# Kernel optimization log

Measured on AMD Instinct MI355X. Metric: run time of the kernel, lower is better.

## Reference

```python
import jax, jax.numpy as jnp
import numpy as np
import math

N_HEAD = 16

def setup_inputs() -> dict:
    key = jax.random.key(0)
    ks = jax.random.split(key, 8)
    B, S, P, NX = 4, 1024, 128, 1024
    return {
        "x": jax.random.normal(ks[0], (B, S, NX), jnp.float32),
        "M": jax.random.normal(ks[1], (B, P, NX), jnp.float32),
        "Mmask": jnp.ones((B, P), jnp.float32),
        "attention_mask": jnp.zeros((B, 1, 1, S), jnp.float32),
        "W_attn": jax.random.normal(ks[2], (NX, 3 * NX), jnp.float32) * 0.02,
        "b_attn": jnp.zeros((3 * NX,), jnp.float32),
        "W_mem": jax.random.normal(ks[3], (NX, 2 * NX), jnp.float32) * 0.02,
        "b_mem": jnp.zeros((2 * NX,), jnp.float32),
        "W_proj": jax.random.normal(ks[4], (NX, NX), jnp.float32) * 0.02,
        "b_proj": jnp.zeros((NX,), jnp.float32),
    }

def _split_heads(t, H):
    B, T, NX = t.shape
    return t.reshape(B, T, H, NX // H).transpose(0, 2, 1, 3)  # [B,H,T,dh]

def reference(x, M, Mmask, attention_mask, W_attn, b_attn, W_mem, b_mem, W_proj, b_proj):
    B, S, NX = x.shape
    H = N_HEAD
    dh = NX // H
    P = M.shape[1]

    # fused QKV projection (Conv1D == x @ W + b)
    qkv = x @ W_attn + b_attn
    q, k, v = jnp.split(qkv, 3, axis=2)

    # memory K/V projection, prepended along the key/value sequence axis
    ekv = M @ W_mem + b_mem
    ek, ev = jnp.split(ekv, 2, axis=2)
    key = jnp.concatenate([ek, k], axis=1)   # [B, P+S, NX]
    value = jnp.concatenate([ev, v], axis=1)

    qh = _split_heads(q, H)      # [B,H,S,dh]
    kh = _split_heads(key, H)    # [B,H,P+S,dh]
    vh = _split_heads(value, H)  # [B,H,P+S,dh]

    w = jnp.einsum('bhsd,bhtd->bhst', qh, kh) / math.sqrt(dh)  # [B,H,S,P+S]

    # causal bias over the self part, all-ones over the memory part
    causal = jnp.tril(jnp.ones((S, S), w.dtype))
    b = jnp.concatenate([jnp.ones((S, P), w.dtype), causal], axis=1)[None, None]  # [1,1,S,P+S]
    w = w * b - 10000.0 * (1.0 - b)

    # additive attention mask: memory-mask bias concatenated before token mask
    mem_bias = (1.0 - Mmask)[:, None, None, :] * -10000.0  # [B,1,1,P]
    am = jnp.concatenate([mem_bias, jnp.broadcast_to(attention_mask, (B, 1, 1, S))], axis=3)
    w = w + am

    w = jax.nn.softmax(w, axis=-1)
    a = jnp.einsum('bhst,bhtd->bhsd', w, vh)                  # [B,H,S,dh]
    a = a.transpose(0, 2, 1, 3).reshape(B, S, NX)             # merge heads
    return a @ W_proj + b_proj
```

## Files before the change

### kernel.cpp

```cpp
#include <hip/hip_runtime.h>
#include <hip/hip_bf16.h>


typedef __attribute__((ext_vector_type(8))) short bf16x8;
typedef __attribute__((ext_vector_type(4))) float f32x4;

#define MFMA16(a, b, c) __builtin_amdgcn_mfma_f32_16x16x32_bf16((a), (b), (c), 0, 0, 0)

#define GLOAD_LDS16(g, l)                                                  \
    __builtin_amdgcn_global_load_lds(                                      \
        (const __attribute__((address_space(1))) void*)(const void*)(g),   \
        (__attribute__((address_space(3))) void*)(void*)(l), 16, 0, 0)

static __device__ __forceinline__ unsigned short f2bf(float f) {
    union { float f; unsigned int u; } v; v.f = f;
    unsigned int u = v.u;
    return (unsigned short)((u + 0x7fffu + ((u >> 16) & 1u)) >> 16);
}

static __device__ __forceinline__ void transpose_body(const float* __restrict__ W,
                                                      unsigned short* __restrict__ Wt,
                                                      int K, int N, int bx, int by,
                                                      float (*tile)[33]) {
    int n0 = bx * 32, k0 = by * 32;
    int tx = threadIdx.x & 31, ty = threadIdx.x >> 5;
    #pragma unroll
    for (int r = ty; r < 32; r += 8) tile[r][tx] = W[(size_t)(k0 + r) * N + n0 + tx];
    __syncthreads();
    #pragma unroll
    for (int r = ty; r < 32; r += 8) Wt[(size_t)(n0 + r) * K + k0 + tx] = f2bf(tile[tx][r]);
}

__global__ void prep_all(const float* __restrict__ x, const float* __restrict__ Mem,
                         unsigned short* __restrict__ x_bf, unsigned short* __restrict__ M_bf,
                         const float* __restrict__ W_attn, const float* __restrict__ W_mem,
                         const float* __restrict__ W_proj, unsigned short* __restrict__ Wat,
                         unsigned short* __restrict__ Wmt, unsigned short* __restrict__ Wpt,
                         const float* __restrict__ Mmask, const float* __restrict__ amask,
                         float* __restrict__ biasT) {
    __shared__ float tile[32][33];
    int bid = blockIdx.x;
    if (bid < 4608) {
        int i = bid * 256 + threadIdx.x;
        if (i < 1048576) {
            float4 v = ((const float4*)x)[i];
            ushort4 o; o.x = f2bf(v.x); o.y = f2bf(v.y); o.z = f2bf(v.z); o.w = f2bf(v.w);
            ((ushort4*)x_bf)[i] = o;
        } else {
            int j = i - 1048576;
            float4 v = ((const float4*)Mem)[j];
            ushort4 o; o.x = f2bf(v.x); o.y = f2bf(v.y); o.z = f2bf(v.z); o.w = f2bf(v.w);
            ((ushort4*)M_bf)[j] = o;
        }
        return;
    }
    bid -= 4608;
    if (bid < 3072) {
        transpose_body(W_attn, Wat, 1024, 3072, bid % 96, bid / 96, tile);
    } else if (bid < 5120) {
        int t = bid - 3072; transpose_body(W_mem, Wmt, 1024, 2048, t % 64, t / 64, tile);
    } else if (bid < 6144) {
        int t = bid - 5120; transpose_body(W_proj, Wpt, 1024, 1024, t % 32, t / 32, tile);
    } else {
        int i = (bid - 6144) * 256 + threadIdx.x;
        if (i < 4 * 1152) {
            int b = i / 1152, t = i % 1152;
            float v = (t < 128) ? (Mmask[b * 128 + t] - 1.f) * 10000.f
                                : amask[b * 1024 + t - 128];
            biasT[i] = v * 1.4426950408889634f;
        }
    }
}

__global__ __launch_bounds__(256, 4) void gemm_fused(
        const unsigned short* __restrict__ x_bf, const unsigned short* __restrict__ Wat,
        const float* __restrict__ b_attn, const unsigned short* __restrict__ M_bf,
        const unsigned short* __restrict__ Wmt, const float* __restrict__ b_mem,
        unsigned short* __restrict__ Qbuf, unsigned short* __restrict__ Kc,
        unsigned short* __restrict__ Vt) {
    __shared__ char smem[34816];
    unsigned short* As = (unsigned short*)smem;
    unsigned short* Bs = (unsigned short*)(smem + 8192);
    const int tid = threadIdx.x;
    const int lane = tid & 63, wave = tid >> 6;
    const int quad = lane >> 4, l16 = lane & 15;
    const int crow = lane >> 2, ccol = (lane & 3) * 8;
    const int bid = blockIdx.x;

    if (bid < 768) {
        const int bm = bid & 31, bn = bid >> 5;
        const int wm = (wave & 1) * 64, wn = (wave >> 1) * 64;
        const unsigned short* Abase = x_bf + (size_t)(bm * 128 + crow) * 1024 + ccol;
        const unsigned short* Bbase = Wat + (size_t)(bn * 128 + crow) * 1024 + ccol;
        f32x4 acc[4][4] = {};
        for (int k0 = 0; k0 < 1024; k0 += 32) {
            __syncthreads();
            #pragma unroll
            for (int cc = 0; cc < 4; cc++) {
                const int c = wave * 4 + cc;
                if (c < 8) GLOAD_LDS16(Abase + (size_t)(c * 16) * 1024 + k0, &As[c * 512]);
                else       GLOAD_LDS16(Bbase + (size_t)((c - 8) * 16) * 1024 + k0, &Bs[(c - 8) * 512]);
            }
            __syncthreads();
            bf16x8 af[4], bf[4];
            #pragma unroll
            for (int i = 0; i < 4; i++) af[i] = *(const bf16x8*)&As[(wm + i * 16 + l16) * 32 + quad * 8];
            #pragma unroll
            for (int j = 0; j < 4; j++) bf[j] = *(const bf16x8*)&Bs[(wn + j * 16 + l16) * 32 + quad * 8];
            #pragma unroll
            for (int i = 0; i < 4; i++)
                #pragma unroll
                for (int j = 0; j < 4; j++)
                    acc[i][j] = MFMA16(af[i], bf[j], acc[i][j]);
        }
        float bj[4];
        #pragma unroll
        for (int j = 0; j < 4; j++) bj[j] = b_attn[bn * 128 + wn + j * 16 + l16];
        __syncthreads();
        if (bn < 8) {
            #pragma unroll
            for (int i = 0; i < 4; i++) {
                const int row = bm * 128 + wm + i * 16 + quad * 4;
                #pragma unroll
                for (int j = 0; j < 4; j++) {
                    const int col = bn * 128 + wn + j * 16 + l16;
                    #pragma unroll
                    for (int r = 0; r < 4; r++)
                        Qbuf[(size_t)(row + r) * 1024 + col] = f2bf(acc[i][j][r] + bj[j]);
                }
            }
        } else if (bn < 16) {
            #pragma unroll
            for (int i = 0; i < 4; i++) {
                const int row = bm * 128 + wm + i * 16 + quad * 4;
                const int b = row >> 10, s = row & 1023;
                #pragma unroll
                for (int j = 0; j < 4; j++) {
                    const int c = bn * 128 + wn + j * 16 + l16 - 1024;
                    unsigned short* kd = Kc + (size_t)((b << 4) | (c >> 6)) * 73728 +
                                         (size_t)(s + 128) * 64 + (c & 63);
                    #pragma unroll
                    for (int r = 0; r < 4; r++) kd[(size_t)r * 64] = f2bf(acc[i][j][r] + bj[j]);
                }
            }
        } else {
            unsigned short* Tw = (unsigned short*)smem + wave * 4352;
            #pragma unroll
            for (int i = 0; i < 4; i++)
                #pragma unroll
                for (int j = 0; j < 4; j++)
                    #pragma unroll
                    for (int r = 0; r < 4; r++)
                        Tw[(j * 16 + l16) * 68 + i * 16 + quad * 4 + r] = f2bf(acc[i][j][r] + bj[j]);
            const int vb = (bn - 16) * 128 + wn;
            const int h = vb >> 6;
            const int b = bm >> 3, s0 = (bm * 128 + wm) & 1023;
            unsigned short* vd = Vt + (size_t)((b << 4) | h) * 73728 +
                                 (size_t)lane * 1152 + 128 + s0;
            #pragma unroll
            for (int ch = 0; ch < 8; ch++)
                *(bf16x8*)(vd + ch * 8) = *(const bf16x8*)&Tw[lane * 68 + ch * 8];
        }
    } else {
        const int t = bid - 768;
        const int bm = t >> 5, bn = t & 31;
        const int wm = (wave & 1) * 32, wn = (wave >> 1) * 32;
        const unsigned short* Abase = M_bf + (size_t)(bm * 64 + crow) * 1024 + ccol;
        const unsigned short* Bbase = Wmt + (size_t)(bn * 64 + crow) * 1024 + ccol;
        f32x4 acc[2][2] = {};
        for (int k0 = 0; k0 < 1024; k0 += 32) {
            __syncthreads();
            #pragma unroll
            for (int cc = 0; cc < 2; cc++) {
                const int c = wave * 2 + cc;
                if (c < 4) GLOAD_LDS16(Abase + (size_t)(c * 16) * 1024 + k0, &As[c * 512]);
                else       GLOAD_LDS16(Bbase + (size_t)((c - 4) * 16) * 1024 + k0, &Bs[(c - 4) * 512]);
            }
            __syncthreads();
            bf16x8 af[2], bf[2];
            #pragma unroll
            for (int i = 0; i < 2; i++) af[i] = *(const bf16x8*)&As[(wm + i * 16 + l16) * 32 + quad * 8];
            #pragma unroll
            for (int j = 0; j < 2; j++) bf[j] = *(const bf16x8*)&Bs[(wn + j * 16 + l16) * 32 + quad * 8];
            #pragma unroll
            for (int i = 0; i < 2; i++)
                #pragma unroll
                for (int j = 0; j < 2; j++)
                    acc[i][j] = MFMA16(af[i], bf[j], acc[i][j]);
        }
        float bj[2];
        #pragma unroll
        for (int j = 0; j < 2; j++) bj[j] = b_mem[bn * 64 + wn + j * 16 + l16];
        __syncthreads();
        if (bn < 16) {
            #pragma unroll
            for (int i = 0; i < 2; i++) {
                const int row = bm * 64 + wm + i * 16 + quad * 4;
                const int b = row >> 7, p = row & 127;
                #pragma unroll
                for (int j = 0; j < 2; j++) {
                    const int c = bn * 64 + wn + j * 16 + l16;
                    unsigned short* kd = Kc + (size_t)((b << 4) | (c >> 6)) * 73728 +
                                         (size_t)p * 64 + (c & 63);
                    #pragma unroll
                    for (int r = 0; r < 4; r++) kd[(size_t)r * 64] = f2bf(acc[i][j][r] + bj[j]);
                }
            }
        } else {
            unsigned short* Tw = (unsigned short*)smem + wave * 1152;
            #pragma unroll
            for (int i = 0; i < 2; i++)
                #pragma unroll
                for (int j = 0; j < 2; j++)
                    #pragma unroll
                    for (int r = 0; r < 4; r++)
                        Tw[(j * 16 + l16) * 36 + i * 16 + quad * 4 + r] = f2bf(acc[i][j][r] + bj[j]);
            const int vb = bn * 64 + wn - 1024;
            const int h = vb >> 6, d0 = vb & 63;
            const int b = (bm * 64 + wm) >> 7, p0 = (bm * 64 + wm) & 127;
            const int lc = lane >> 1, half = lane & 1;
            unsigned short* vd = Vt + (size_t)((b << 4) | h) * 73728 +
                                 (size_t)(d0 + lc) * 1152 + p0 + half * 16;
            #pragma unroll
            for (int ch = 0; ch < 2; ch++)
                *(bf16x8*)(vd + ch * 8) = *(const bf16x8*)&Tw[lc * 36 + half * 16 + ch * 8];
        }
    }
}

__global__ __launch_bounds__(256) void attn_kernel(const unsigned short* __restrict__ Qbuf,
                                                   const unsigned short* __restrict__ Kc,
                                                   const unsigned short* __restrict__ Vt,
                                                   const float* __restrict__ biasT,
                                                   unsigned short* __restrict__ Aout) {
    __shared__ unsigned short Ks[2 * 64 * 32];
    __shared__ unsigned short Vs[2 * 64 * 32];
    __shared__ unsigned short Ps[4][16 * 72];
    const int tid = threadIdx.x;
    const int lane = tid & 63, wave = tid >> 6;
    const int quad = lane >> 4, l16 = lane & 15;
    const int blk = blockIdx.x;
    const int xcd = blk & 7, idx = blk >> 3;
    const int bh = xcd * 8 + (idx >> 4);
    const int qg = 15 - (idx & 15);
    const int h = bh & 15, b = bh >> 4;
    const int qrow0 = qg * 64;
    const int qrow_w = qrow0 + wave * 16;

    bf16x8 qf[2];
    #pragma unroll
    for (int k2 = 0; k2 < 2; k2++)
        qf[k2] = *(const bf16x8*)(Qbuf + (size_t)(b * 1024 + qrow_w + l16) * 1024 +
                                  h * 64 + k2 * 32 + quad * 8);

    const unsigned short* Kb = Kc + (size_t)bh * 73728;
    const unsigned short* Vb = Vt + (size_t)bh * 73728;
    const float* bias_b = biasT + b * 1152;

    const int srow = lane >> 2;
    const int sc8 = (lane & 3) * 8;

    bf16x8 ones;
    #pragma unroll
    for (int j = 0; j < 8; j++) ones[j] = (short)0x3F80;

    f32x4 o[4] = {};
    f32x4 oden = {};
    const int tmax = min(1152, qrow0 + 192);

    for (int t0 = 0; t0 < tmax; t0 += 64) {
        __syncthreads();
        #pragma unroll
        for (int cc = 0; cc < 4; cc++) {
            const int c = wave * 4 + cc;
            if (c < 8) {
                const int kk = c & 1, rch = c >> 1;
                GLOAD_LDS16(Kb + (size_t)(t0 + rch * 16 + srow) * 64 + kk * 32 + sc8,
                            &Ks[kk * 2048 + rch * 512]);
            } else {
                const int c2 = c - 8, tk = c2 & 1, dch = c2 >> 1;
                GLOAD_LDS16(Vb + (size_t)(dch * 16 + srow) * 1152 + t0 + tk * 32 + sc8,
                            &Vs[tk * 2048 + dch * 512]);
            }
        }
        __syncthreads();
        if (t0 <= qrow_w + 143) {
            const bool nomask = (t0 + 63 <= 128 + qrow_w);
            float4 bt[4];
            #pragma unroll
            for (int tn = 0; tn < 4; tn++)
                bt[tn] = *(const float4*)(bias_b + t0 + tn * 16 + quad * 4);
            const int sg = qrow_w + l16;
            #pragma unroll
            for (int tn = 0; tn < 4; tn++) {
                bf16x8 kf0 = *(const bf16x8*)&Ks[0 * 2048 + (tn * 16 + l16) * 32 + quad * 8];
                bf16x8 kf1 = *(const bf16x8*)&Ks[1 * 2048 + (tn * 16 + l16) * 32 + quad * 8];
                f32x4 st = {};
                st = MFMA16(kf0, qf[0], st);
                st = MFMA16(kf1, qf[1], st);
                float p[4];
                #pragma unroll
                for (int r = 0; r < 4; r++) {
                    float e = __builtin_amdgcn_exp2f(st[r] * 0.18033688011112042f + bt[tn][r]);
                    if (!nomask) {
                        const int tg = t0 + tn * 16 + quad * 4 + r;
                        e = (tg < 128 || tg - 128 <= sg) ? e : 0.f;
                    }
                    p[r] = e;
                }
                union { ushort4 u; __hip_bfloat162 h2[2]; } pk;
                pk.h2[0] = __float22bfloat162_rn(float2{p[0], p[1]});
                pk.h2[1] = __float22bfloat162_rn(float2{p[2], p[3]});
                *(ushort4*)&Ps[wave][l16 * 72 + tn * 16 + quad * 4] = pk.u;
            }
            #pragma unroll
            for (int tk = 0; tk < 2; tk++) {
                bf16x8 pf = *(const bf16x8*)&Ps[wave][l16 * 72 + tk * 32 + quad * 8];
                oden = MFMA16(pf, ones, oden);
                #pragma unroll
                for (int dn = 0; dn < 4; dn++) {
                    bf16x8 vf = *(const bf16x8*)&Vs[tk * 2048 + (dn * 16 + l16) * 32 + quad * 8];
                    o[dn] = MFMA16(pf, vf, o[dn]);
                }
            }
        }
    }

    #pragma unroll
    for (int r = 0; r < 4; r++) {
        const float inv = 1.f / oden[r];
        const size_t orow = (size_t)(b * 1024 + qrow_w + quad * 4 + r) * 1024 + h * 64;
        #pragma unroll
        for (int dn = 0; dn < 4; dn++)
            Aout[orow + dn * 16 + l16] = f2bf(o[dn][r] * inv);
    }
}

__global__ __launch_bounds__(256) void gemm_proj(const unsigned short* __restrict__ Abuf,
                                                 const unsigned short* __restrict__ Wpt,
                                                 const float* __restrict__ b_proj,
                                                 float* __restrict__ out) {
    __shared__ unsigned short As[128 * 32];
    __shared__ unsigned short Bs[64 * 32];
    const int tid = threadIdx.x;
    const int lane = tid & 63, wave = tid >> 6;
    const int quad = lane >> 4, l16 = lane & 15;
    const int wm = (wave & 1) * 64, wn = (wave >> 1) * 32;
    const int bm = blockIdx.x & 31, bn = blockIdx.x >> 5;
    const int crow = lane >> 2, ccol = (lane & 3) * 8;
    const unsigned short* Abase = Abuf + (size_t)(bm * 128 + crow) * 1024 + ccol;
    const unsigned short* Bbase = Wpt + (size_t)(bn * 64 + crow) * 1024 + ccol;

    f32x4 acc[4][2] = {};
    for (int k0 = 0; k0 < 1024; k0 += 32) {
        __syncthreads();
        #pragma unroll
        for (int cc = 0; cc < 3; cc++) {
            const int c = wave * 3 + cc;
            if (c < 8) GLOAD_LDS16(Abase + (size_t)(c * 16) * 1024 + k0, &As[c * 512]);
            else if (c < 12) GLOAD_LDS16(Bbase + (size_t)((c - 8) * 16) * 1024 + k0, &Bs[(c - 8) * 512]);
        }
        __syncthreads();
        bf16x8 af[4], bf[2];
        #pragma unroll
        for (int i = 0; i < 4; i++) af[i] = *(const bf16x8*)&As[(wm + i * 16 + l16) * 32 + quad * 8];
        #pragma unroll
        for (int j = 0; j < 2; j++) bf[j] = *(const bf16x8*)&Bs[(wn + j * 16 + l16) * 32 + quad * 8];
        #pragma unroll
        for (int i = 0; i < 4; i++)
            #pragma unroll
            for (int j = 0; j < 2; j++)
                acc[i][j] = MFMA16(af[i], bf[j], acc[i][j]);
    }
    float bj[2];
    #pragma unroll
    for (int j = 0; j < 2; j++) bj[j] = b_proj[bn * 64 + wn + j * 16 + l16];
    #pragma unroll
    for (int i = 0; i < 4; i++) {
        const int row = bm * 128 + wm + i * 16 + quad * 4;
        #pragma unroll
        for (int j = 0; j < 2; j++) {
            const int col = bn * 64 + wn + j * 16 + l16;
            #pragma unroll
            for (int r = 0; r < 4; r++)
                out[(size_t)(row + r) * 1024 + col] = acc[i][j][r] + bj[j];
        }
    }
}

extern "C" void kernel_launch(void* const* d_in, const int* in_sizes, int n_in,
                              void* d_out, int out_size, void* d_ws, size_t ws_size,
                              hipStream_t stream) {
    const float* x      = (const float*)d_in[0];
    const float* Mem    = (const float*)d_in[1];
    const float* Mmask  = (const float*)d_in[2];
    const float* amask  = (const float*)d_in[3];
    const float* W_attn = (const float*)d_in[4];
    const float* b_attn = (const float*)d_in[5];
    const float* W_mem  = (const float*)d_in[6];
    const float* b_mem  = (const float*)d_in[7];
    const float* W_proj = (const float*)d_in[8];
    const float* b_proj = (const float*)d_in[9];
    float* out = (float*)d_out;

    char* ws = (char*)d_ws;
    unsigned short* x_bf  = (unsigned short*)ws;  ws += (size_t)4096 * 1024 * 2;
    unsigned short* M_bf  = (unsigned short*)ws;  ws += (size_t)512 * 1024 * 2;
    unsigned short* Wat   = (unsigned short*)ws;  ws += (size_t)3072 * 1024 * 2;
    unsigned short* Wmt   = (unsigned short*)ws;  ws += (size_t)2048 * 1024 * 2;
    unsigned short* Wpt   = (unsigned short*)ws;  ws += (size_t)1024 * 1024 * 2;
    unsigned short* Qbuf  = (unsigned short*)ws;  ws += (size_t)4096 * 1024 * 2;
    unsigned short* Abuf  = (unsigned short*)ws;  ws += (size_t)4096 * 1024 * 2;
    unsigned short* Kc    = (unsigned short*)ws;  ws += (size_t)64 * 1152 * 64 * 2;
    unsigned short* Vt    = (unsigned short*)ws;  ws += (size_t)64 * 64 * 1152 * 2;
    float*          biasT = (float*)ws;           ws += (size_t)4 * 1152 * 4;

    prep_all<<<10771, 256, 0, stream>>>(x, Mem, x_bf, M_bf, W_attn, W_mem, W_proj,
                                        Wat, Wmt, Wpt, Mmask, amask, biasT);
    gemm_fused<<<1024, 256, 0, stream>>>(x_bf, Wat, b_attn, M_bf, Wmt, b_mem,
                                         Qbuf, Kc, Vt);
    attn_kernel<<<1024, 256, 0, stream>>>(Qbuf, Kc, Vt, biasT, Abuf);
    gemm_proj<<<512, 256, 0, stream>>>(Abuf, Wpt, b_proj, out);
}
```

Before: 209.4 us.

## Shrink attention blocks to two waves with paired causal query tiles and swizzled LDS

The attention kernel now launches 128-thread blocks, each handling two 32-row query tiles from opposite ends of the causal range (pair and 31-pair), so per-block work is balanced. K/V tiles are loaded whole by one wave each into 64x64 LDS arrays with an XOR swizzle on the column chunk to avoid bank conflicts. Smaller blocks raise occupancy but halve the reuse of each K/V tile across query rows, so more global/LDS traffic per query.

```diff
diff --git a/kernel.cpp b/kernel.cpp
--- a/kernel.cpp
+++ b/kernel.cpp
@@ -228,111 +228,116 @@
     }
 }
 
-__global__ __launch_bounds__(256) void attn_kernel(const unsigned short* __restrict__ Qbuf,
+__global__ __launch_bounds__(128) void attn_kernel(const unsigned short* __restrict__ Qbuf,
                                                    const unsigned short* __restrict__ Kc,
                                                    const unsigned short* __restrict__ Vt,
                                                    const float* __restrict__ biasT,
                                                    unsigned short* __restrict__ Aout) {
-    __shared__ unsigned short Ks[2 * 64 * 32];
-    __shared__ unsigned short Vs[2 * 64 * 32];
-    __shared__ unsigned short Ps[4][16 * 72];
+    __shared__ unsigned short Ks[64 * 64];
+    __shared__ unsigned short Vs[64 * 64];
+    __shared__ unsigned short Ps[2][16 * 72];
     const int tid = threadIdx.x;
     const int lane = tid & 63, wave = tid >> 6;
     const int quad = lane >> 4, l16 = lane & 15;
     const int blk = blockIdx.x;
     const int xcd = blk & 7, idx = blk >> 3;
-    const int bh = xcd * 8 + (idx >> 4);
-    const int qg = 15 - (idx & 15);
+    const int bh = xcd * 8 + (idx & 7);
+    const int pair = idx >> 3;
     const int h = bh & 15, b = bh >> 4;
-    const int qrow0 = qg * 64;
-    const int qrow_w = qrow0 + wave * 16;
-
-    bf16x8 qf[2];
-    #pragma unroll
-    for (int k2 = 0; k2 < 2; k2++)
-        qf[k2] = *(const bf16x8*)(Qbuf + (size_t)(b * 1024 + qrow_w + l16) * 1024 +
-                                  h * 64 + k2 * 32 + quad * 8);
 
     const unsigned short* Kb = Kc + (size_t)bh * 73728;
     const unsigned short* Vb = Vt + (size_t)bh * 73728;
     const float* bias_b = biasT + b * 1152;
 
-    const int srow = lane >> 2;
-    const int sc8 = (lane & 3) * 8;
+    const int srow = lane >> 3;
+    const int scol = ((lane & 7) ^ srow) * 8;
+    const int rswz = l16 & 7;
 
     bf16x8 ones;
     #pragma unroll
     for (int j = 0; j < 8; j++) ones[j] = (short)0x3F80;
 
-    f32x4 o[4] = {};
-    f32x4 oden = {};
-    const int tmax = min(1152, qrow0 + 192);
-
-    for (int t0 = 0; t0 < tmax; t0 += 64) {
-        __syncthreads();
-        #pragma unroll
-        for (int cc = 0; cc < 4; cc++) {
-            const int c = wave * 4 + cc;
-            if (c < 8) {
-                const int kk = c & 1, rch = c >> 1;
-                GLOAD_LDS16(Kb + (size_t)(t0 + rch * 16 + srow) * 64 + kk * 32 + sc8,
-                            &Ks[kk * 2048 + rch * 512]);
+    #pragma unroll
+    for (int phase = 0; phase < 2; phase++) {
+        const int qg = phase ? (31 - pair) : pair;
+        const int qrow0 = qg * 32;
+        const int qrow_w = qrow0 + wave * 16;
+
+        bf16x8 qf[2];
+        #pragma unroll
+        for (int k2 = 0; k2 < 2; k2++)
+            qf[k2] = *(const bf16x8*)(Qbuf + (size_t)(b * 1024 + qrow_w + l16) * 1024 +
+                                      h * 64 + k2 * 32 + quad * 8);
+
+        f32x4 o[4] = {};
+        f32x4 oden = {};
+        const int tmax = min(1152, ((qrow0 + 223) >> 6) << 6);
+
+        for (int t0 = 0; t0 < tmax; t0 += 64) {
+            __syncthreads();
+            if (wave == 0) {
+                const unsigned short* g = Kb + (size_t)(t0 + srow) * 64 + scol;
+                #pragma unroll
+                for (int ch = 0; ch < 8; ch++)
+                    GLOAD_LDS16(g + (size_t)(ch * 8) * 64, &Ks[ch * 512]);
             } else {
-                const int c2 = c - 8, tk = c2 & 1, dch = c2 >> 1;
-                GLOAD_LDS16(Vb + (size_t)(dch * 16 + srow) * 1152 + t0 + tk * 32 + sc8,
-                            &Vs[tk * 2048 + dch * 512]);
-            }
-        }
-        __syncthreads();
-        if (t0 <= qrow_w + 143) {
-            const bool nomask = (t0 + 63 <= 128 + qrow_w);
-            float4 bt[4];
-            #pragma unroll
-            for (int tn = 0; tn < 4; tn++)
-                bt[tn] = *(const float4*)(bias_b + t0 + tn * 16 + quad * 4);
-            const int sg = qrow_w + l16;
-            #pragma unroll
-            for (int tn = 0; tn < 4; tn++) {
-                bf16x8 kf0 = *(const bf16x8*)&Ks[0 * 2048 + (tn * 16 + l16) * 32 + quad * 8];
-                bf16x8 kf1 = *(const bf16x8*)&Ks[1 * 2048 + (tn * 16 + l16) * 32 + quad * 8];
-                f32x4 st = {};
-                st = MFMA16(kf0, qf[0], st);
-                st = MFMA16(kf1, qf[1], st);
-                float p[4];
-                #pragma unroll
-                for (int r = 0; r < 4; r++) {
-                    float e = __builtin_amdgcn_exp2f(st[r] * 0.18033688011112042f + bt[tn][r]);
-                    if (!nomask) {
-                        const int tg = t0 + tn * 16 + quad * 4 + r;
-                        e = (tg < 128 || tg - 128 <= sg) ? e : 0.f;
+                const unsigned short* g = Vb + (size_t)srow * 1152 + t0 + scol;
+                #pragma unroll
+                for (int ch = 0; ch < 8; ch++)
+                    GLOAD_LDS16(g + (size_t)(ch * 8) * 1152, &Vs[ch * 512]);
+            }
+            __syncthreads();
+            if (t0 <= qrow_w + 143) {
+                const bool nomask = (t0 + 63 <= 128 + qrow_w);
+                float4 bt[4];
+                #pragma unroll
+                for (int tn = 0; tn < 4; tn++)
+                    bt[tn] = *(const float4*)(bias_b + t0 + tn * 16 + quad * 4);
+                const int sg = qrow_w + l16;
+                #pragma unroll
+                for (int tn = 0; tn < 4; tn++) {
+                    bf16x8 kf0 = *(const bf16x8*)&Ks[(tn * 16 + l16) * 64 + (quad ^ rswz) * 8];
+                    bf16x8 kf1 = *(const bf16x8*)&Ks[(tn * 16 + l16) * 64 + ((quad + 4) ^ rswz) * 8];
+                    f32x4 st = {};
+                    st = MFMA16(kf0, qf[0], st);
+                    st = MFMA16(kf1, qf[1], st);
+                    float p[4];
+                    #pragma unroll
+                    for (int r = 0; r < 4; r++) {
+                        float e = __builtin_amdgcn_exp2f(st[r] * 0.18033688011112042f + bt[tn][r]);
+                        if (!nomask) {
+                            const int tg = t0 + tn * 16 + quad * 4 + r;
+                            e = (tg < 128 || tg - 128 <= sg) ? e : 0.f;
+                        }
+                        p[r] = e;
                     }
-                    p[r] = e;
+                    union { ushort4 u; __hip_bfloat162 h2[2]; } pk;
+                    pk.h2[0] = __float22bfloat162_rn(float2{p[0], p[1]});
+                    pk.h2[1] = __float22bfloat162_rn(float2{p[2], p[3]});
+                    *(ushort4*)&Ps[wave][l16 * 72 + tn * 16 + quad * 4] = pk.u;
                 }
-                union { ushort4 u; __hip_bfloat162 h2[2]; } pk;
-                pk.h2[0] = __float22bfloat162_rn(float2{p[0], p[1]});
-                pk.h2[1] = __float22bfloat162_rn(float2{p[2], p[3]});
-                *(ushort4*)&Ps[wave][l16 * 72 + tn * 16 + quad * 4] = pk.u;
-            }
-            #pragma unroll
-            for (int tk = 0; tk < 2; tk++) {
-                bf16x8 pf = *(const bf16x8*)&Ps[wave][l16 * 72 + tk * 32 + quad * 8];
-                oden = MFMA16(pf, ones, oden);
-                #pragma unroll
-                for (int dn = 0; dn < 4; dn++) {
-                    bf16x8 vf = *(const bf16x8*)&Vs[tk * 2048 + (dn * 16 + l16) * 32 + quad * 8];
-                    o[dn] = MFMA16(pf, vf, o[dn]);
+                #pragma unroll
+                for (int tk = 0; tk < 2; tk++) {
+                    bf16x8 pf = *(const bf16x8*)&Ps[wave][l16 * 72 + tk * 32 + quad * 8];
+                    oden = MFMA16(pf, ones, oden);
+                    #pragma unroll
+                    for (int dn = 0; dn < 4; dn++) {
+                        bf16x8 vf = *(const bf16x8*)&Vs[(dn * 16 + l16) * 64 +
+                                                        ((tk * 4 + quad) ^ rswz) * 8];
+                        o[dn] = MFMA16(pf, vf, o[dn]);
+                    }
                 }
             }
         }
-    }
-
-    #pragma unroll
-    for (int r = 0; r < 4; r++) {
-        const float inv = 1.f / oden[r];
-        const size_t orow = (size_t)(b * 1024 + qrow_w + quad * 4 + r) * 1024 + h * 64;
-        #pragma unroll
-        for (int dn = 0; dn < 4; dn++)
-            Aout[orow + dn * 16 + l16] = f2bf(o[dn][r] * inv);
+
+        #pragma unroll
+        for (int r = 0; r < 4; r++) {
+            const float inv = 1.f / oden[r];
+            const size_t orow = (size_t)(b * 1024 + qrow_w + quad * 4 + r) * 1024 + h * 64;
+            #pragma unroll
+            for (int dn = 0; dn < 4; dn++)
+                Aout[orow + dn * 16 + l16] = f2bf(o[dn][r] * inv);
+        }
     }
 }
 
@@ -419,6 +424,6 @@
                                         Wat, Wmt, Wpt, Mmask, amask, biasT);
     gemm_fused<<<1024, 256, 0, stream>>>(x_bf, Wat, b_attn, M_bf, Wmt, b_mem,
                                          Qbuf, Kc, Vt);
-    attn_kernel<<<1024, 256, 0, stream>>>(Qbuf, Kc, Vt, biasT, Abuf);
+    attn_kernel<<<1024, 128, 0, stream>>>(Qbuf, Kc, Vt, biasT, Abuf);
     gemm_proj<<<512, 256, 0, stream>>>(Abuf, Wpt, b_proj, out);
 }
```

Result: faster. 199.4 us (-4.8%).
